# Performance work log

Measured on AMD Instinct MI355X. Metric: run time of the kernel, lower is better.

## Reference

```python
import jax, jax.numpy as jnp
import numpy as np

B, NS, NT = 8, 1024, 1024
SRC, TGT, OUT, H = 1024, 1024, 1024, 8
DH = OUT // H  # per-head dim = 128


def setup_inputs() -> dict:
    key = jax.random.key(0)
    ks = jax.random.split(key, 9)
    s = 0.02
    return {
        "src": jax.random.normal(ks[0], (B, NS, SRC), jnp.float32),
        "tgt": jax.random.normal(ks[1], (B, NT, TGT), jnp.float32),
        "src_mask": jnp.ones((B, NS), jnp.float32),
        "tgt_mask": jnp.ones((B, NT), jnp.float32),
        "Ws": jax.random.normal(ks[2], (2 * OUT, SRC), jnp.float32) * s,
        "bs": jnp.zeros((2 * OUT,), jnp.float32),
        "Wt": jax.random.normal(ks[3], (OUT, TGT), jnp.float32) * s,
        "bt": jnp.zeros((OUT,), jnp.float32),
        "Wo": jax.random.normal(ks[4], (OUT, OUT + TGT), jnp.float32) * s,
        "bo": jnp.zeros((OUT,), jnp.float32),
    }


def reference(src, tgt, src_mask, tgt_mask, Ws, bs, Wt, bt, Wo, bo):
    # src_lin / tgt_lin (FCNet = linear, no activation, drop=0 at eval)
    src_trans = jnp.einsum("bsf,of->bso", src, Ws) + bs  # [B,NS,2*OUT]
    tgt_trans = jnp.einsum("btf,of->bto", tgt, Wt) + bt  # [B,NT,OUT]
    src_trans = src_trans * src_mask[:, :, None]
    tgt_trans = tgt_trans * tgt_mask[:, :, None]

    src_key, src_val = jnp.split(src_trans, 2, axis=2)  # each [B,NS,OUT]
    # head split along channels == reshape to [.., H, DH]
    k = src_key.reshape(B, NS, H, DH)
    v = src_val.reshape(B, NS, H, DH)
    q = tgt_trans.reshape(B, NT, H, DH)

    scores = jnp.einsum("bthd,bshd->bhts", q, k) / jnp.sqrt(jnp.float32(DH))
    scores = jnp.where(src_mask[:, None, None, :] == 0, -jnp.inf, scores)
    attn = jax.nn.softmax(scores, axis=-1)  # [B,H,NT,NS]
    tgt_update = jnp.einsum("bhts,bshd->bthd", attn, v).reshape(B, NT, OUT)

    cat_tgt = jnp.concatenate([tgt, tgt_update], axis=2)  # [B,NT,TGT+OUT]
    update_tgt = jnp.einsum("btf,of->bto", cat_tgt, Wo) + bo
    return update_tgt
```

## Files before the change

### kernel.cpp

```cpp
#include <hip/hip_runtime.h>


typedef __bf16 bf16x8 __attribute__((ext_vector_type(8)));
typedef float f32x4 __attribute__((ext_vector_type(4)));
typedef unsigned short u16;
typedef unsigned short u16x8 __attribute__((ext_vector_type(8)));

#define MFMA16(a, b, c) __builtin_amdgcn_mfma_f32_16x16x32_bf16((a), (b), (c), 0, 0, 0)

__device__ __forceinline__ float bf2f(u16 b) {
  return __uint_as_float(((unsigned)b) << 16);
}
__device__ __forceinline__ u16 f2bf(float f) {
  unsigned u = __float_as_uint(f);
  u += 0x7fffu + ((u >> 16) & 1u);
  return (u16)(u >> 16);
}
__device__ __forceinline__ u16 f2bf_hw(float f) {
  __bf16 h = (__bf16)f;
  return __builtin_bit_cast(u16, h);
}

__device__ __forceinline__ void async16(const u16* g, u16* l) {
  __builtin_amdgcn_global_load_lds(
      (const __attribute__((address_space(1))) unsigned int*)g,
      (__attribute__((address_space(3))) unsigned int*)l, 16, 0, 0);
}

struct Cvt5 {
  const float* src[5];
  unsigned cnt4[5];
  unsigned ooff[5];
};

__global__ __launch_bounds__(256)
void cvt5_kernel(Cvt5 a, u16* __restrict__ out, unsigned total4)
{
  unsigned gid = blockIdx.x * 256u + threadIdx.x;
  if (gid >= total4) return;
  unsigned rem = gid;
  int s = 0;
  while (s < 4 && rem >= a.cnt4[s]) { rem -= a.cnt4[s]; ++s; }
  const float4 v = ((const float4*)a.src[s])[rem];
  ushort4 o;
  o.x = f2bf(v.x); o.y = f2bf(v.y); o.z = f2bf(v.z); o.w = f2bf(v.w);
  *(ushort4*)(out + a.ooff[s] + (size_t)rem * 4) = o;
}

template <int MODE, typename OutT>
__global__ __launch_bounds__(256, 2)
void gemm_bt_kernel(const u16* __restrict__ A0, const u16* __restrict__ A1,
                    int splitK,
                    const u16* __restrict__ Bw, const float* __restrict__ bias,
                    const float* __restrict__ rowscale,
                    OutT* __restrict__ C, int N, int K)
{
  __shared__ u16 As[128 * 32];
  __shared__ u16 Bs[128 * 32];
  const int tid  = threadIdx.x;
  const int lane = tid & 63;
  const int w    = tid >> 6;
  const int wm = w >> 1, wn = w & 1;
  const int quad = lane >> 4, lr = lane & 15;
  const unsigned nwg  = gridDim.x * gridDim.y;
  const unsigned wgid = blockIdx.y * gridDim.x + blockIdx.x;
  const unsigned swz  = (wgid & 7u) * (nwg >> 3) + (wgid >> 3);
  const int m0 = (int)(swz / gridDim.x) * 128;
  const int n0 = (int)(swz % gridDim.x) * 128;

  const f32x4 z4 = {0.f, 0.f, 0.f, 0.f};
  f32x4 acc[4][4];
#pragma unroll
  for (int i = 0; i < 4; ++i)
#pragma unroll
    for (int j = 0; j < 4; ++j)
      acc[i][j] = z4;

  const int acol = (tid & 3) * 8;

  for (int k0 = 0; k0 < K; k0 += 32) {
    const u16* Ap; int lda, kk;
    if (k0 < splitK) { Ap = A0; lda = splitK;     kk = k0; }
    else             { Ap = A1; lda = K - splitK; kk = k0 - splitK; }
    __syncthreads();
#pragma unroll
    for (int it = 0; it < 2; ++it) {
      const int row = it * 64 + (tid >> 2);
      const int ldsbase = (it * 256 + (tid & 192)) * 8;
      async16(Ap + (size_t)(m0 + row) * lda + (kk + acol), &As[ldsbase]);
      async16(Bw + (size_t)(n0 + row) * K   + (k0 + acol), &Bs[ldsbase]);
    }
    __syncthreads();

    bf16x8 af[4], bfr[4];
#pragma unroll
    for (int i = 0; i < 4; ++i)
      af[i] = *(const bf16x8*)&As[(wm * 64 + i * 16 + lr) * 32 + quad * 8];
#pragma unroll
    for (int j = 0; j < 4; ++j)
      bfr[j] = *(const bf16x8*)&Bs[(wn * 64 + j * 16 + lr) * 32 + quad * 8];
#pragma unroll
    for (int i = 0; i < 4; ++i)
#pragma unroll
      for (int j = 0; j < 4; ++j)
        acc[i][j] = MFMA16(af[i], bfr[j], acc[i][j]);
  }

  float bv[4];
#pragma unroll
  for (int j = 0; j < 4; ++j)
    bv[j] = bias[n0 + wn * 64 + j * 16 + lr];

#pragma unroll
  for (int i = 0; i < 4; ++i)
#pragma unroll
    for (int r = 0; r < 4; ++r) {
      const int grow = m0 + wm * 64 + i * 16 + quad * 4 + r;
      float rs = 1.f;
      if (rowscale) rs = rowscale[grow];
#pragma unroll
      for (int j = 0; j < 4; ++j) {
        const int gcol = n0 + wn * 64 + j * 16 + lr;
        const float val = (acc[i][j][r] + bv[j]) * rs;
        if (MODE == 0) {
          C[(size_t)grow * N + gcol] = (OutT)val;
        } else {
          const int b = grow >> 10, s = grow & 1023;
          size_t off;
          if (gcol < 1024) {
            const int h = gcol >> 7, d = gcol & 127;
            off = ((((size_t)(b * 8 + h) * 16 + (d >> 3)) * 1024 + s) * 8) + (d & 7);
          } else {
            const int cc = gcol - 1024;
            const int h = cc >> 7, d = cc & 127;
            off = (size_t)8388608 +
                  ((((size_t)(b * 8 + h) * 16 + (s >> 6)) * 1024 +
                    ((s >> 3) & 7) * 128 + d) * 8) + (s & 7);
          }
          ((u16*)C)[off] = f2bf(val);
        }
      }
    }
}

template <>
__global__ __launch_bounds__(256, 2)
void gemm_bt_kernel<0, u16>(const u16* __restrict__ A0, const u16* __restrict__ A1,
                            int splitK,
                            const u16* __restrict__ Bw, const float* __restrict__ bias,
                            const float* __restrict__ rowscale,
                            u16* __restrict__ C, int N, int K)
{
  __shared__ u16 As[128 * 32];
  __shared__ u16 Bs[128 * 32];
  const int tid  = threadIdx.x;
  const int lane = tid & 63;
  const int w    = tid >> 6;
  const int wm = w >> 1, wn = w & 1;
  const int quad = lane >> 4, lr = lane & 15;
  const unsigned nwg  = gridDim.x * gridDim.y;
  const unsigned wgid = blockIdx.y * gridDim.x + blockIdx.x;
  const unsigned swz  = (wgid & 7u) * (nwg >> 3) + (wgid >> 3);
  const int m0 = (int)(swz / gridDim.x) * 128;
  const int n0 = (int)(swz % gridDim.x) * 128;

  const f32x4 z4 = {0.f, 0.f, 0.f, 0.f};
  f32x4 acc[4][4];
#pragma unroll
  for (int i = 0; i < 4; ++i)
#pragma unroll
    for (int j = 0; j < 4; ++j)
      acc[i][j] = z4;

  const int acol = (tid & 3) * 8;

  for (int k0 = 0; k0 < K; k0 += 32) {
    const u16* Ap; int lda, kk;
    if (k0 < splitK) { Ap = A0; lda = splitK;     kk = k0; }
    else             { Ap = A1; lda = K - splitK; kk = k0 - splitK; }
    __syncthreads();
#pragma unroll
    for (int it = 0; it < 2; ++it) {
      const int row = it * 64 + (tid >> 2);
      const int ldsbase = (it * 256 + (tid & 192)) * 8;
      async16(Ap + (size_t)(m0 + row) * lda + (kk + acol), &As[ldsbase]);
      async16(Bw + (size_t)(n0 + row) * K   + (k0 + acol), &Bs[ldsbase]);
    }
    __syncthreads();

    bf16x8 af[4], bfr[4];
#pragma unroll
    for (int i = 0; i < 4; ++i)
      af[i] = *(const bf16x8*)&As[(wm * 64 + i * 16 + lr) * 32 + quad * 8];
#pragma unroll
    for (int j = 0; j < 4; ++j)
      bfr[j] = *(const bf16x8*)&Bs[(wn * 64 + j * 16 + lr) * 32 + quad * 8];
#pragma unroll
    for (int i = 0; i < 4; ++i)
#pragma unroll
      for (int j = 0; j < 4; ++j)
        acc[i][j] = MFMA16(af[i], bfr[j], acc[i][j]);
  }

  float bv[4];
#pragma unroll
  for (int j = 0; j < 4; ++j)
    bv[j] = bias[n0 + wn * 64 + j * 16 + lr];

#pragma unroll
  for (int i = 0; i < 4; ++i)
#pragma unroll
    for (int r = 0; r < 4; ++r) {
      const int grow = m0 + wm * 64 + i * 16 + quad * 4 + r;
      float rs = 1.f;
      if (rowscale) rs = rowscale[grow];
#pragma unroll
      for (int j = 0; j < 4; ++j) {
        const int gcol = n0 + wn * 64 + j * 16 + lr;
        C[(size_t)grow * N + gcol] = f2bf((acc[i][j][r] + bv[j]) * rs);
      }
    }
}

#define SCLOG2E 0.12751813754618667f

__global__ __launch_bounds__(256, 2)
void flash_kernel(const u16* __restrict__ q, const u16* __restrict__ Kg,
                  const u16* __restrict__ Vg,
                  const float* __restrict__ smask, u16* __restrict__ upd)
{
  __shared__ u16 Ks[64 * 128];
  __shared__ u16 Vs[64 * 128];
  __shared__ u16 Ps[4][2 * 16 * 64];

  const int tid  = threadIdx.x;
  const int lane = tid & 63;
  const int w    = tid >> 6;
  const int quad = lane >> 4, lr = lane & 15;
  const int bh_i = blockIdx.x;
  const int qt   = blockIdx.y;
  const int b = bh_i >> 3, h = bh_i & 7;
  const size_t bh = (size_t)bh_i;

  const size_t qrow0 = (size_t)b * 1024 + qt * 128 + w * 16;

  bf16x8 qf[2][4];
#pragma unroll
  for (int s = 0; s < 2; ++s)
#pragma unroll
    for (int kk = 0; kk < 4; ++kk)
      qf[s][kk] = *(const bf16x8*)
          &q[(qrow0 + s * 64 + lr) * 1024 + h * 128 + kk * 32 + quad * 8];

  const f32x4 z4 = {0.f, 0.f, 0.f, 0.f};
  f32x4 oacc[2][8];
#pragma unroll
  for (int s = 0; s < 2; ++s)
#pragma unroll
    for (int jd = 0; jd < 8; ++jd) oacc[s][jd] = z4;
  float lsum[2][4] = {{0.f, 0.f, 0.f, 0.f}, {0.f, 0.f, 0.f, 0.f}};

  for (int s0 = 0; s0 < 1024; s0 += 64) {
    const int t = s0 >> 6;
    __syncthreads();
#pragma unroll
    for (int it = 0; it < 4; ++it) {
      const int dc = it * 4 + w;
      async16(Kg + (((bh * 16 + dc) * 1024) + s0 + lane) * 8,
              &Ks[(it * 256 + (tid & 192)) * 8]);
    }
#pragma unroll
    for (int it = 0; it < 4; ++it) {
      const int f = it * 256 + tid;
      async16(Vg + ((bh * 16 + t) * 1024 + f) * 8,
              &Vs[(it * 256 + (tid & 192)) * 8]);
    }
    __syncthreads();

    f32x4 sacc[2][4];
#pragma unroll
    for (int s = 0; s < 2; ++s)
#pragma unroll
      for (int j = 0; j < 4; ++j) sacc[s][j] = z4;
    __builtin_amdgcn_s_setprio(1);
#pragma unroll
    for (int kk = 0; kk < 4; ++kk) {
      bf16x8 kb[4];
#pragma unroll
      for (int j = 0; j < 4; ++j)
        kb[j] = *(const bf16x8*)&Ks[((kk * 4 + quad) * 64 + j * 16 + lr) * 8];
#pragma unroll
      for (int s = 0; s < 2; ++s)
#pragma unroll
        for (int j = 0; j < 4; ++j)
          sacc[s][j] = MFMA16(qf[s][kk], kb[j], sacc[s][j]);
    }
    __builtin_amdgcn_s_setprio(0);

    float mb[4];
#pragma unroll
    for (int j = 0; j < 4; ++j) {
      const float mv = smask[b * 1024 + s0 + j * 16 + lr];
      mb[j] = (mv == 0.f) ? -1e30f : 0.f;
    }

#pragma unroll
    for (int s = 0; s < 2; ++s)
#pragma unroll
      for (int r = 0; r < 4; ++r) {
        const int row = quad * 4 + r;
        const int rsw = (row & 7) * 8;
        float ps = 0.f;
#pragma unroll
        for (int j = 0; j < 4; ++j) {
          const float p = exp2f(fmaf(sacc[s][j][r], SCLOG2E, mb[j]));
          ps += p;
          Ps[w][s * 1024 + row * 64 + ((j * 16 + lr) ^ rsw)] = f2bf_hw(p);
        }
        lsum[s][r] += ps;
      }

    __builtin_amdgcn_s_setprio(1);
#pragma unroll
    for (int kk2 = 0; kk2 < 2; ++kk2) {
      bf16x8 pa[2], vb[8];
#pragma unroll
      for (int s = 0; s < 2; ++s)
        pa[s] = *(const bf16x8*)
            &Ps[w][s * 1024 + lr * 64 + ((kk2 * 32 + quad * 8) ^ ((lr & 7) * 8))];
#pragma unroll
      for (int jd = 0; jd < 8; ++jd)
        vb[jd] = *(const bf16x8*)&Vs[((kk2 * 4 + quad) * 128 + jd * 16 + lr) * 8];
#pragma unroll
      for (int s = 0; s < 2; ++s)
#pragma unroll
        for (int jd = 0; jd < 8; ++jd)
          oacc[s][jd] = MFMA16(pa[s], vb[jd], oacc[s][jd]);
    }
    __builtin_amdgcn_s_setprio(0);
  }

#pragma unroll
  for (int s = 0; s < 2; ++s)
#pragma unroll
    for (int r = 0; r < 4; ++r) {
      float l = lsum[s][r];
      l += __shfl_xor(l, 1);
      l += __shfl_xor(l, 2);
      l += __shfl_xor(l, 4);
      l += __shfl_xor(l, 8);
      const float inv = 1.f / l;
      const size_t grow = qrow0 + s * 64 + quad * 4 + r;
#pragma unroll
      for (int jd = 0; jd < 8; ++jd)
        upd[grow * 1024 + h * 128 + jd * 16 + lr] = f2bf_hw(oacc[s][jd][r] * inv);
    }
}

__global__ void magic_kernel(float* out, float val)
{
  if (threadIdx.x == 0 && blockIdx.x == 0) out[0] = val;
}

extern "C" void kernel_launch(void* const* d_in, const int* in_sizes, int n_in,
                              void* d_out, int out_size, void* d_ws, size_t ws_size,
                              hipStream_t stream)
{
  static const int dict_sz[10]   = {8388608, 8388608, 8192, 8192, 2097152,
                                    2048, 1048576, 1024, 2097152, 1024};
  static const int sorted_sz[10] = {2097152, 2097152, 1048576, 1024, 2048,
                                    1024, 8388608, 8192, 8388608, 8192};
  bool is_dict = (n_in == 10), is_sorted = (n_in == 10);
  if (n_in == 10) {
    for (int i = 0; i < 10; ++i) {
      if (in_sizes[i] != dict_sz[i])   is_dict = false;
      if (in_sizes[i] != sorted_sz[i]) is_sorted = false;
    }
  }

  const float *src, *tgt, *smask, *tmask, *Ws, *bs, *Wt, *bt, *Wo, *bo;
  if (is_sorted) {
    Wo    = (const float*)d_in[0];
    Ws    = (const float*)d_in[1];
    Wt    = (const float*)d_in[2];
    bo    = (const float*)d_in[3];
    bs    = (const float*)d_in[4];
    bt    = (const float*)d_in[5];
    src   = (const float*)d_in[6];
    smask = (const float*)d_in[7];
    tgt   = (const float*)d_in[8];
    tmask = (const float*)d_in[9];
  } else {
    src   = (const float*)d_in[0];
    tgt   = (const float*)d_in[1];
    smask = (const float*)d_in[2];
    tmask = (const float*)d_in[3];
    Ws    = (const float*)d_in[4];
    bs    = (const float*)d_in[5];
    Wt    = (const float*)d_in[6];
    bt    = (const float*)d_in[7];
    Wo    = (const float*)d_in[8];
    bo    = (const float*)d_in[9];
  }
  float* out = (float*)d_out;

  const size_t KV = 16777216, Q = 8388608, UPD = 8388608;
  const unsigned segsz[5] = {8388608u, 8388608u, 2097152u, 1048576u, 2097152u};
  size_t total_u16 = KV + Q + UPD;
  unsigned aoff[5], off = 0, total4 = 0;
  for (int i = 0; i < 5; ++i) {
    aoff[i] = off;
    off += segsz[i];
    total4 += segsz[i] / 4u;
  }
  total_u16 += off;

  unsigned ws_mb = (unsigned)(ws_size >> 20);
  if (ws_mb > 999u) ws_mb = 999u;
  if (!is_dict && !is_sorted) {
    magic_kernel<<<dim3(1), dim3(64), 0, stream>>>(out, 4000.f + (float)ws_mb);
    return;
  }
  if (ws_size < total_u16 * 2) {
    magic_kernel<<<dim3(1), dim3(64), 0, stream>>>(out, 3000.f + (float)ws_mb);
    return;
  }

  u16* kvbuf  = (u16*)d_ws;
  u16* qbuf   = kvbuf + KV;
  u16* updbuf = qbuf + Q;
  u16* arena  = updbuf + UPD;

  Cvt5 ca;
  const float* segp[5] = {src, tgt, Ws, Wt, Wo};
  for (int i = 0; i < 5; ++i) {
    ca.src[i]  = segp[i];
    ca.cnt4[i] = segsz[i] / 4u;
    ca.ooff[i] = aoff[i];
  }
  const u16* srcb = arena + aoff[0];
  const u16* tgtb = arena + aoff[1];
  const u16* Wsb  = arena + aoff[2];
  const u16* Wtb  = arena + aoff[3];
  const u16* Wob  = arena + aoff[4];

  dim3 blk(256);
  cvt5_kernel<<<dim3((total4 + 255u) / 256u), blk, 0, stream>>>(ca, arena, total4);
  gemm_bt_kernel<1, u16><<<dim3(16, 64), blk, 0, stream>>>(
      srcb, nullptr, 1024, Wsb, bs, smask, kvbuf, 2048, 1024);
  gemm_bt_kernel<0, u16><<<dim3(8, 64), blk, 0, stream>>>(
      tgtb, nullptr, 1024, Wtb, bt, tmask, qbuf, 1024, 1024);
  flash_kernel<<<dim3(64, 8), blk, 0, stream>>>(
      qbuf, kvbuf, kvbuf + 8388608, smask, updbuf);
  gemm_bt_kernel<0, float><<<dim3(8, 64), blk, 0, stream>>>(
      tgtb, updbuf, 1024, Wob, bo, nullptr, out, 1024, 2048);
}
```

Before: 313.2 us.

## Stage K/V GEMM epilogue through LDS for coalesced stores, split K loop

```diff
diff --git a/kernel.cpp b/kernel.cpp
--- a/kernel.cpp
+++ b/kernel.cpp
@@ -48,7 +48,7 @@
 }
 
 template <int MODE, typename OutT>
-__global__ __launch_bounds__(256, 2)
+__global__ __launch_bounds__(256, 3)
 void gemm_bt_kernel(const u16* __restrict__ A0, const u16* __restrict__ A1,
                     int splitK,
                     const u16* __restrict__ Bw, const float* __restrict__ bias,
@@ -78,10 +78,7 @@
 
   const int acol = (tid & 3) * 8;
 
-  for (int k0 = 0; k0 < K; k0 += 32) {
-    const u16* Ap; int lda, kk;
-    if (k0 < splitK) { Ap = A0; lda = splitK;     kk = k0; }
-    else             { Ap = A1; lda = K - splitK; kk = k0 - splitK; }
+  auto kstep = [&](const u16* Ap, int lda, int kk, int k0) {
     __syncthreads();
 #pragma unroll
     for (int it = 0; it < 2; ++it) {
@@ -104,47 +101,80 @@
 #pragma unroll
       for (int j = 0; j < 4; ++j)
         acc[i][j] = MFMA16(af[i], bfr[j], acc[i][j]);
-  }
+  };
+
+  for (int k0 = 0; k0 < splitK; k0 += 32) kstep(A0, splitK, k0, k0);
+  for (int k0 = splitK; k0 < K; k0 += 32) kstep(A1, K - splitK, k0 - splitK, k0);
 
   float bv[4];
 #pragma unroll
   for (int j = 0; j < 4; ++j)
     bv[j] = bias[n0 + wn * 64 + j * 16 + lr];
 
-#pragma unroll
-  for (int i = 0; i < 4; ++i)
-#pragma unroll
-    for (int r = 0; r < 4; ++r) {
-      const int grow = m0 + wm * 64 + i * 16 + quad * 4 + r;
-      float rs = 1.f;
-      if (rowscale) rs = rowscale[grow];
-#pragma unroll
-      for (int j = 0; j < 4; ++j) {
-        const int gcol = n0 + wn * 64 + j * 16 + lr;
-        const float val = (acc[i][j][r] + bv[j]) * rs;
-        if (MODE == 0) {
-          C[(size_t)grow * N + gcol] = (OutT)val;
-        } else {
-          const int b = grow >> 10, s = grow & 1023;
-          size_t off;
-          if (gcol < 1024) {
-            const int h = gcol >> 7, d = gcol & 127;
-            off = ((((size_t)(b * 8 + h) * 16 + (d >> 3)) * 1024 + s) * 8) + (d & 7);
-          } else {
-            const int cc = gcol - 1024;
-            const int h = cc >> 7, d = cc & 127;
-            off = (size_t)8388608 +
-                  ((((size_t)(b * 8 + h) * 16 + (s >> 6)) * 1024 +
-                    ((s >> 3) & 7) * 128 + d) * 8) + (s & 7);
-          }
-          ((u16*)C)[off] = f2bf(val);
+  if constexpr (MODE == 0) {
+#pragma unroll
+    for (int i = 0; i < 4; ++i)
+#pragma unroll
+      for (int r = 0; r < 4; ++r) {
+        const int grow = m0 + wm * 64 + i * 16 + quad * 4 + r;
+        float rs = 1.f;
+        if (rowscale) rs = rowscale[grow];
+#pragma unroll
+        for (int j = 0; j < 4; ++j) {
+          const int gcol = n0 + wn * 64 + j * 16 + lr;
+          C[(size_t)grow * N + gcol] = (OutT)((acc[i][j][r] + bv[j]) * rs);
         }
       }
-    }
+  } else {
+    __shared__ u16 kvtile[16384];
+    const int bb  = m0 >> 10;
+    const int s0b = m0 & 1023;
+    const bool isK = (n0 < 1024);
+    const int h = isK ? (n0 >> 7) : ((n0 - 1024) >> 7);
+    const size_t bh = (size_t)(bb * 8 + h);
+
+#pragma unroll
+    for (int i = 0; i < 4; ++i)
+#pragma unroll
+      for (int r = 0; r < 4; ++r) {
+        const int sl = wm * 64 + i * 16 + quad * 4 + r;
+        float rs = 1.f;
+        if (rowscale) rs = rowscale[m0 + sl];
+#pragma unroll
+        for (int j = 0; j < 4; ++j) {
+          const int d = wn * 64 + j * 16 + lr;
+          const float val = (acc[i][j][r] + bv[j]) * rs;
+          int addr;
+          if (isK) {
+            addr = ((d >> 3) * 128 + sl) * 8 + (d & 7);
+          } else {
+            addr = (sl >> 6) * 8192 + (((sl >> 3) & 7) * 128 + d) * 8 + (sl & 7);
+          }
+          kvtile[addr] = f2bf(val);
+        }
+      }
+    __syncthreads();
+
+    const size_t gbase = isK
+        ? (bh * 131072 + (size_t)s0b * 8)
+        : ((size_t)8388608 + bh * 131072 + (size_t)(s0b >> 6) * 8192);
+#pragma unroll
+    for (int it = 0; it < 8; ++it) {
+      const int idx = it * 256 + tid;
+      size_t dst;
+      if (isK) {
+        const int dc = idx >> 7;
+        dst = gbase + (size_t)dc * 8192 + (size_t)(idx & 127) * 8;
+      } else {
+        dst = gbase + (size_t)idx * 8;
+      }
+      *(u16x8*)((u16*)C + dst) = *(const u16x8*)&kvtile[idx * 8];
+    }
+  }
 }
 
 template <>
-__global__ __launch_bounds__(256, 2)
+__global__ __launch_bounds__(256, 3)
 void gemm_bt_kernel<0, u16>(const u16* __restrict__ A0, const u16* __restrict__ A1,
                             int splitK,
                             const u16* __restrict__ Bw, const float* __restrict__ bias,
@@ -174,10 +204,7 @@
 
   const int acol = (tid & 3) * 8;
 
-  for (int k0 = 0; k0 < K; k0 += 32) {
-    const u16* Ap; int lda, kk;
-    if (k0 < splitK) { Ap = A0; lda = splitK;     kk = k0; }
-    else             { Ap = A1; lda = K - splitK; kk = k0 - splitK; }
+  auto kstep = [&](const u16* Ap, int lda, int kk, int k0) {
     __syncthreads();
 #pragma unroll
     for (int it = 0; it < 2; ++it) {
@@ -200,7 +227,10 @@
 #pragma unroll
       for (int j = 0; j < 4; ++j)
         acc[i][j] = MFMA16(af[i], bfr[j], acc[i][j]);
-  }
+  };
+
+  for (int k0 = 0; k0 < splitK; k0 += 32) kstep(A0, splitK, k0, k0);
+  for (int k0 = splitK; k0 < K; k0 += 32) kstep(A1, K - splitK, k0 - splitK, k0);
 
   float bv[4];
 #pragma unroll
```

After: 317.7 us. About the same (+1.5%).
